# Optimization experiments

Hardware: AMD Instinct MI355X
Metric: run time of the kernel (lower is better)

The kernel has to match this reference:

```python
import jax, jax.numpy as jnp
import numpy as np
from jax import lax

STORAGE = 8
HIDDEN_HEAD = 32
N_BLOCKS = 16


def _conv(x, w, b, padding):
    # x: NCHW, w: OIHW
    y = lax.conv_general_dilated(
        x, w, window_strides=(1, 1), padding=padding,
        dimension_numbers=("NCHW", "OIHW", "NCHW"))
    return y + b[None, :, None, None]


def _min_pool3(x):
    # 3x3 sliding-window min, stride 1, same padding (pad value +inf so it
    return lax.reduce_window(x, float("inf"), lax.min,
                             (1, 1, 3, 3), (1, 1, 1, 1), "SAME")


def setup_inputs() -> dict:
    key = jax.random.key(0)
    ks = jax.random.split(key, 7)
    B, H, W = 8, 512, 512
    x = jax.random.normal(ks[0], (B, 1, H, W), dtype=jnp.float32)
    # initial 1x1 conv: 1 -> 8
    w0 = jax.random.normal(ks[1], (STORAGE, 1, 1, 1), dtype=jnp.float32) * 1.0
    b0 = jax.random.normal(ks[2], (STORAGE,), dtype=jnp.float32) * 0.1
    # head conv 3x3: 8 -> 32
    w1 = jax.random.normal(ks[3], (HIDDEN_HEAD, STORAGE, 3, 3), dtype=jnp.float32) * (1.0 / np.sqrt(STORAGE * 9))
    b1 = jax.random.normal(ks[4], (HIDDEN_HEAD,), dtype=jnp.float32) * 0.1
    # head conv 1x1: 32 -> 1
    w2 = jax.random.normal(ks[5], (1, HIDDEN_HEAD, 1, 1), dtype=jnp.float32) * (1.0 / np.sqrt(HIDDEN_HEAD))
    b2 = jax.random.normal(ks[6], (1,), dtype=jnp.float32) * 0.1
    return {"x": x, "w0": w0, "b0": b0, "w1": w1, "b1": b1, "w2": w2, "b2": b2}


def reference(x, w0, b0, w1, b1, w2, b2):
    h = _conv(x, w0, b0, "SAME")  # [B,8,H,W]
    for _ in range(N_BLOCKS):
        h = h + _min_pool3(h)
    h = _conv(h, w1, b1, "SAME")  # [B,32,H,W]
    h = jax.nn.relu(h)
    return _conv(h, w2, b2, "SAME")  # [B,1,H,W]
```

## Files before the change

### kernel.cpp

```cpp
#include <hip/hip_runtime.h>
#include <math.h>


#define N_PIX (512*512)
#define INF __builtin_inff()

typedef __attribute__((ext_vector_type(2))) float f2;

__device__ __forceinline__ float dpp_shr1(float v, float fill) {
    return __int_as_float(__builtin_amdgcn_update_dpp(
        __float_as_int(fill), __float_as_int(v), 0x138, 0xF, 0xF, false));
}
__device__ __forceinline__ float dpp_shl1(float v, float fill) {
    return __int_as_float(__builtin_amdgcn_update_dpp(
        __float_as_int(fill), __float_as_int(v), 0x130, 0xF, 0xF, false));
}

struct Row8 { float4 a, b; };

__device__ __forceinline__ Row8 row_update8(const Row8 up, const Row8 mid, const Row8 dn)
{
    float4 va, vb;
    va.x = fminf(fminf(up.a.x, mid.a.x), dn.a.x);
    va.y = fminf(fminf(up.a.y, mid.a.y), dn.a.y);
    va.z = fminf(fminf(up.a.z, mid.a.z), dn.a.z);
    va.w = fminf(fminf(up.a.w, mid.a.w), dn.a.w);
    vb.x = fminf(fminf(up.b.x, mid.b.x), dn.b.x);
    vb.y = fminf(fminf(up.b.y, mid.b.y), dn.b.y);
    vb.z = fminf(fminf(up.b.z, mid.b.z), dn.b.z);
    vb.w = fminf(fminf(up.b.w, mid.b.w), dn.b.w);
    float vmL = dpp_shr1(vb.w, INF);
    float vmR = dpp_shl1(va.x, INF);
    float tm1 = fminf(vmL, va.x);
    float t0 = fminf(va.x, va.y), t1 = fminf(va.y, va.z);
    float t2 = fminf(va.z, va.w), t3 = fminf(va.w, vb.x);
    float t4 = fminf(vb.x, vb.y), t5 = fminf(vb.y, vb.z);
    float t6 = fminf(vb.z, vb.w), t7 = fminf(vb.w, vmR);
    Row8 o;
    o.a.x = mid.a.x + fminf(tm1, t0);
    o.a.y = mid.a.y + fminf(t0, t1);
    o.a.z = mid.a.z + fminf(t1, t2);
    o.a.w = mid.a.w + fminf(t2, t3);
    o.b.x = mid.b.x + fminf(t3, t4);
    o.b.y = mid.b.y + fminf(t4, t5);
    o.b.z = mid.b.z + fminf(t5, t6);
    o.b.w = mid.b.w + fminf(t6, t7);
    return o;
}

__device__ __forceinline__ void halo_write(float* hp, const Row8& v) {
    hp[0*64]=v.a.x; hp[1*64]=v.a.y; hp[2*64]=v.a.z; hp[3*64]=v.a.w;
    hp[4*64]=v.b.x; hp[5*64]=v.b.y; hp[6*64]=v.b.z; hp[7*64]=v.b.w;
}
__device__ __forceinline__ Row8 halo_read(const float* hp) {
    Row8 v;
    v.a.x=hp[0*64]; v.a.y=hp[1*64]; v.a.z=hp[2*64]; v.a.w=hp[3*64];
    v.b.x=hp[4*64]; v.b.y=hp[5*64]; v.b.z=hp[6*64]; v.b.w=hp[7*64];
    return v;
}

__global__ __launch_bounds__(512, 2) void erode16_kernel(
    const float* __restrict__ x, float* __restrict__ A,
    const float* __restrict__ w0, const float* __restrict__ b0,
    const float* __restrict__ w1, const float* __restrict__ b1,
    float* __restrict__ W)
{
    if (blockIdx.x == 0 && blockIdx.y == 0 && threadIdx.x < 288) {
        int tid = threadIdx.x;
        int oc = tid / 9, k = tid - oc*9;
        float wp = 0.f, wq = 0.f;
        for (int ic = 0; ic < 8; ++ic) {
            float a = w0[ic];
            float w = w1[oc*72 + ic*9 + k];
            if (a > 0.f) wp += w * a;
            else         wq += w * (-a);
        }
        W[(oc*9 + k)*2 + 0] = wp;
        W[(oc*9 + k)*2 + 1] = wq;
        if (k == 0) {
            float beta[9];
            for (int kk = 0; kk < 9; ++kk) {
                float s = 0.f;
                for (int ic = 0; ic < 8; ++ic) s += b0[ic] * w1[oc*72 + ic*9 + kk];
                beta[kk] = 65536.0f * s;
            }
            float R[3], L[3], Rr[3];
            for (int r = 0; r < 3; ++r) {
                R[r]  = beta[r*3] + beta[r*3+1] + beta[r*3+2];
                L[r]  = beta[r*3 + 0];
                Rr[r] = beta[r*3 + 2];
            }
            float bb = b1[oc];
            W[576 + 0*96 + oc]      = bb + R[1] + R[2];
            W[576 + 0*96 + 32 + oc] = L[1] + L[2];
            W[576 + 0*96 + 64 + oc] = Rr[1] + Rr[2];
            W[576 + 1*96 + oc]      = bb + R[0] + R[1] + R[2];
            W[576 + 1*96 + 32 + oc] = L[0] + L[1] + L[2];
            W[576 + 1*96 + 64 + oc] = Rr[0] + Rr[1] + Rr[2];
            W[576 + 2*96 + oc]      = bb + R[0] + R[1];
            W[576 + 2*96 + 32 + oc] = L[0] + L[1];
            W[576 + 2*96 + 64 + oc] = Rr[0] + Rr[1];
        }
    }

    __shared__ float halo[2][8][4][8][64];
    const int tid   = threadIdx.x;
    const int lane  = tid & 63;
    const int w     = tid >> 6;
    const int ty    = blockIdx.x;
    const int plane = blockIdx.y;
    const int colg  = lane * 8;
    const int row0g = ty*32 - 16 + w*8;

    const float* sp = x + (plane & 7)*N_PIX;
    const float sgn = (plane >= 8) ? -1.f : 1.f;

    Row8 h[8];
    #pragma unroll
    for (int r = 0; r < 8; ++r) {
        int gy = row0g + r;
        if ((unsigned)gy < 512u) {
            const float* rp = sp + gy*512 + colg;
            float4 a = *(const float4*)rp;
            float4 b = *(const float4*)(rp + 4);
            h[r].a = make_float4(a.x*sgn, a.y*sgn, a.z*sgn, a.w*sgn);
            h[r].b = make_float4(b.x*sgn, b.y*sgn, b.z*sgn, b.w*sgn);
        } else {
            h[r].a = make_float4(INF, INF, INF, INF);
            h[r].b = h[r].a;
        }
    }

    const Row8 inf8 = { make_float4(INF,INF,INF,INF), make_float4(INF,INF,INF,INF) };
    for (int s = 0; s < 8; ++s) {
        int par = s & 1;
        halo_write(&halo[par][w][0][0][lane], h[0]);
        halo_write(&halo[par][w][1][0][lane], h[1]);
        halo_write(&halo[par][w][2][0][lane], h[6]);
        halo_write(&halo[par][w][3][0][lane], h[7]);
        Row8 n2 = row_update8(h[1], h[2], h[3]);
        Row8 n3 = row_update8(h[2], h[3], h[4]);
        Row8 n4 = row_update8(h[3], h[4], h[5]);
        Row8 n5 = row_update8(h[4], h[5], h[6]);
        __syncthreads();
        Row8 um2 = inf8, um1 = inf8, dp0 = inf8, dp1 = inf8;
        if (w > 0) {
            um2 = halo_read(&halo[par][w-1][2][0][lane]);
            um1 = halo_read(&halo[par][w-1][3][0][lane]);
        }
        if (w < 7) {
            dp0 = halo_read(&halo[par][w+1][0][0][lane]);
            dp1 = halo_read(&halo[par][w+1][1][0][lane]);
        }
        Row8 nm1 = row_update8(um2, um1, h[0]);
        Row8 n0  = row_update8(um1, h[0], h[1]);
        Row8 n1  = row_update8(h[0], h[1], h[2]);
        Row8 n6  = row_update8(h[5], h[6], h[7]);
        Row8 n7  = row_update8(h[6], h[7], dp0);
        Row8 n8  = row_update8(h[7], dp0, dp1);
        h[0] = row_update8(nm1, n0, n1);
        h[1] = row_update8(n0,  n1, n2);
        h[2] = row_update8(n1,  n2, n3);
        h[3] = row_update8(n2,  n3, n4);
        h[4] = row_update8(n3,  n4, n5);
        h[5] = row_update8(n4,  n5, n6);
        h[6] = row_update8(n5,  n6, n7);
        h[7] = row_update8(n6,  n7, n8);
    }

    if (w >= 2 && w <= 5) {
        float* dp = A + plane*N_PIX;
        #pragma unroll
        for (int r = 0; r < 8; ++r) {
            float* op = dp + (row0g + r)*512 + colg;
            *(float4*)op       = h[r].a;
            *(float4*)(op + 4) = h[r].b;
        }
    }
}

__global__ __launch_bounds__(256) void head_kernel(
    const float* __restrict__ A, const float* __restrict__ W,
    const float* __restrict__ w2, const float* __restrict__ b2,
    float* __restrict__ out)
{
    const int tid  = threadIdx.x;
    const int lane = tid & 63;
    const int w    = tid >> 6;
    const int img  = blockIdx.x >> 7;
    const int y    = (blockIdx.x & 127)*4 + w;
    const int x0   = lane*8;

    const float* P = A + img*N_PIX;
    const float* Q = A + (8 + img)*N_PIX;

    f2 pq[3][10];
    #pragma unroll
    for (int dy = 0; dy < 3; ++dy) {
        int gy = y + dy - 1;
        if ((unsigned)gy < 512u) {
            const float* rp = P + gy*512 + x0;
            const float* rq = Q + gy*512 + x0;
            float4 a = *(const float4*)rp;
            float4 b = *(const float4*)(rp + 4);
            float4 c = *(const float4*)rq;
            float4 d = *(const float4*)(rq + 4);
            pq[dy][1] = (f2){a.x, c.x}; pq[dy][2] = (f2){a.y, c.y};
            pq[dy][3] = (f2){a.z, c.z}; pq[dy][4] = (f2){a.w, c.w};
            pq[dy][5] = (f2){b.x, d.x}; pq[dy][6] = (f2){b.y, d.y};
            pq[dy][7] = (f2){b.z, d.z}; pq[dy][8] = (f2){b.w, d.w};
            pq[dy][0] = (f2){dpp_shr1(b.w, 0.f), dpp_shr1(d.w, 0.f)};
            pq[dy][9] = (f2){dpp_shl1(a.x, 0.f), dpp_shl1(c.x, 0.f)};
        } else {
            #pragma unroll
            for (int j = 0; j < 10; ++j) pq[dy][j] = (f2){0.f, 0.f};
        }
    }

    const int wcase = (y == 0) ? 0 : ((y == 511) ? 2 : 1);
    const float* WB = W + 576 + wcase*96;
    const float mL  = (lane == 0)  ? -1.f : 0.f;
    const float mR  = (lane == 63) ? -1.f : 0.f;

    float o[8];
    #pragma unroll
    for (int j = 0; j < 8; ++j) o[j] = 0.f;

    const f2* Wv = (const f2*)W;
    #pragma unroll 2
    for (int oc = 0; oc < 32; ++oc) {
        f2 acc[8];
        {
            f2 wv0 = Wv[oc*9];
            #pragma unroll
            for (int j = 0; j < 8; ++j) acc[j] = wv0 * pq[0][j];
        }
        #pragma unroll
        for (int t = 1; t < 9; ++t) {
            const int ky = t / 3, kx = t - ky*3;
            f2 wv = Wv[oc*9 + t];
            #pragma unroll
            for (int j = 0; j < 8; ++j) acc[j] += wv * pq[ky][kx + j];
        }
        float base = WB[oc];
        float cl   = WB[32 + oc];
        float cr   = WB[64 + oc];
        float s[8];
        #pragma unroll
        for (int j = 0; j < 8; ++j) s[j] = acc[j].x + acc[j].y + base;
        s[0] = fmaf(cl, mL, s[0]);
        s[7] = fmaf(cr, mR, s[7]);
        float sc = w2[oc];
        #pragma unroll
        for (int j = 0; j < 8; ++j) o[j] += fmaxf(s[j], 0.f) * sc;
    }

    float bb = b2[0];
    float* op = out + img*N_PIX + y*512 + x0;
    *(float4*)(op)     = make_float4(o[0]+bb, o[1]+bb, o[2]+bb, o[3]+bb);
    *(float4*)(op + 4) = make_float4(o[4]+bb, o[5]+bb, o[6]+bb, o[7]+bb);
}

extern "C" void kernel_launch(void* const* d_in, const int* in_sizes, int n_in,
                              void* d_out, int out_size, void* d_ws, size_t ws_size,
                              hipStream_t stream) {
    const float* x  = (const float*)d_in[0];
    const float* w0 = (const float*)d_in[1];
    const float* b0 = (const float*)d_in[2];
    const float* w1 = (const float*)d_in[3];
    const float* b1 = (const float*)d_in[4];
    const float* w2 = (const float*)d_in[5];
    const float* b2 = (const float*)d_in[6];
    float* out = (float*)d_out;

    float* wsf = (float*)d_ws;
    float* A = wsf;
    float* W = wsf + 16*N_PIX;

    dim3 eg(16, 16);
    erode16_kernel<<<eg, 512, 0, stream>>>(x, A, w0, b0, w1, b1, W);

    head_kernel<<<1024, 256, 0, stream>>>(A, W, w2, b2, out);
}
```

Before: 127.8 us.

## Skip dead halo-row erosion work in edge waves and fold head bias into accumulator

In the erosion kernel, the outer waves (0,1,6,7) only feed halo rows to the central output waves, so their updates are now restricted to the shrinking band of rows that still matter at each step. Rows outside that band are skipped while the barriers are kept. The central waves take an unconditional path with no boundary checks, and the wave index is made uniform with readfirstlane. In the head kernel, the bias is split in half, packed as an f2 and folded into the first FMA, which removes one add per pixel per output channel. The cost is extra branching logic in the edge waves and a new weight-table layout.

```diff
diff --git a/kernel.cpp b/kernel.cpp
--- a/kernel.cpp
+++ b/kernel.cpp
@@ -84,33 +84,33 @@
                 for (int ic = 0; ic < 8; ++ic) s += b0[ic] * w1[oc*72 + ic*9 + kk];
                 beta[kk] = 65536.0f * s;
             }
-            float R[3], L[3], Rr[3];
+            float R[3], Lb[3], Rr[3];
             for (int r = 0; r < 3; ++r) {
                 R[r]  = beta[r*3] + beta[r*3+1] + beta[r*3+2];
-                L[r]  = beta[r*3 + 0];
+                Lb[r] = beta[r*3 + 0];
                 Rr[r] = beta[r*3 + 2];
             }
             float bb = b1[oc];
-            W[576 + 0*96 + oc]      = bb + R[1] + R[2];
-            W[576 + 0*96 + 32 + oc] = L[1] + L[2];
-            W[576 + 0*96 + 64 + oc] = Rr[1] + Rr[2];
-            W[576 + 1*96 + oc]      = bb + R[0] + R[1] + R[2];
-            W[576 + 1*96 + 32 + oc] = L[0] + L[1] + L[2];
-            W[576 + 1*96 + 64 + oc] = Rr[0] + Rr[1] + Rr[2];
-            W[576 + 2*96 + oc]      = bb + R[0] + R[1];
-            W[576 + 2*96 + 32 + oc] = L[0] + L[1];
-            W[576 + 2*96 + 64 + oc] = Rr[0] + Rr[1];
+            float Dv[3]  = { bb + R[1] + R[2], bb + R[0] + R[1] + R[2], bb + R[0] + R[1] };
+            float ELv[3] = { Lb[1] + Lb[2], Lb[0] + Lb[1] + Lb[2], Lb[0] + Lb[1] };
+            float ERv[3] = { Rr[1] + Rr[2], Rr[0] + Rr[1] + Rr[2], Rr[0] + Rr[1] };
+            for (int c = 0; c < 3; ++c) {
+                W[576 + (c*32 + oc)*2 + 0] = 0.5f * Dv[c];
+                W[576 + (c*32 + oc)*2 + 1] = 0.5f * Dv[c];
+                W[768 + c*32 + oc] = ELv[c];
+                W[864 + c*32 + oc] = ERv[c];
+            }
         }
     }
 
     __shared__ float halo[2][8][4][8][64];
     const int tid   = threadIdx.x;
     const int lane  = tid & 63;
-    const int w     = tid >> 6;
+    const int wu    = __builtin_amdgcn_readfirstlane(tid >> 6);
     const int ty    = blockIdx.x;
     const int plane = blockIdx.y;
     const int colg  = lane * 8;
-    const int row0g = ty*32 - 16 + w*8;
+    const int row0g = ty*32 - 16 + wu*8;
 
     const float* sp = x + (plane & 7)*N_PIX;
     const float sgn = (plane >= 8) ? -1.f : 1.f;
@@ -132,43 +132,86 @@
     }
 
     const Row8 inf8 = { make_float4(INF,INF,INF,INF), make_float4(INF,INF,INF,INF) };
-    for (int s = 0; s < 8; ++s) {
-        int par = s & 1;
-        halo_write(&halo[par][w][0][0][lane], h[0]);
-        halo_write(&halo[par][w][1][0][lane], h[1]);
-        halo_write(&halo[par][w][2][0][lane], h[6]);
-        halo_write(&halo[par][w][3][0][lane], h[7]);
-        Row8 n2 = row_update8(h[1], h[2], h[3]);
-        Row8 n3 = row_update8(h[2], h[3], h[4]);
-        Row8 n4 = row_update8(h[3], h[4], h[5]);
-        Row8 n5 = row_update8(h[4], h[5], h[6]);
-        __syncthreads();
-        Row8 um2 = inf8, um1 = inf8, dp0 = inf8, dp1 = inf8;
-        if (w > 0) {
-            um2 = halo_read(&halo[par][w-1][2][0][lane]);
-            um1 = halo_read(&halo[par][w-1][3][0][lane]);
-        }
-        if (w < 7) {
-            dp0 = halo_read(&halo[par][w+1][0][0][lane]);
-            dp1 = halo_read(&halo[par][w+1][1][0][lane]);
-        }
-        Row8 nm1 = row_update8(um2, um1, h[0]);
-        Row8 n0  = row_update8(um1, h[0], h[1]);
-        Row8 n1  = row_update8(h[0], h[1], h[2]);
-        Row8 n6  = row_update8(h[5], h[6], h[7]);
-        Row8 n7  = row_update8(h[6], h[7], dp0);
-        Row8 n8  = row_update8(h[7], dp0, dp1);
-        h[0] = row_update8(nm1, n0, n1);
-        h[1] = row_update8(n0,  n1, n2);
-        h[2] = row_update8(n1,  n2, n3);
-        h[3] = row_update8(n2,  n3, n4);
-        h[4] = row_update8(n3,  n4, n5);
-        h[5] = row_update8(n4,  n5, n6);
-        h[6] = row_update8(n5,  n6, n7);
-        h[7] = row_update8(n6,  n7, n8);
-    }
-
-    if (w >= 2 && w <= 5) {
+
+    if (wu >= 2 && wu <= 5) {
+        for (int s = 0; s < 8; ++s) {
+            int par = s & 1;
+            halo_write(&halo[par][wu][0][0][lane], h[0]);
+            halo_write(&halo[par][wu][1][0][lane], h[1]);
+            halo_write(&halo[par][wu][2][0][lane], h[6]);
+            halo_write(&halo[par][wu][3][0][lane], h[7]);
+            Row8 n2 = row_update8(h[1], h[2], h[3]);
+            Row8 n3 = row_update8(h[2], h[3], h[4]);
+            Row8 n4 = row_update8(h[3], h[4], h[5]);
+            Row8 n5 = row_update8(h[4], h[5], h[6]);
+            __syncthreads();
+            Row8 um2 = halo_read(&halo[par][wu-1][2][0][lane]);
+            Row8 um1 = halo_read(&halo[par][wu-1][3][0][lane]);
+            Row8 dp0 = halo_read(&halo[par][wu+1][0][0][lane]);
+            Row8 dp1 = halo_read(&halo[par][wu+1][1][0][lane]);
+            Row8 nm1 = row_update8(um2, um1, h[0]);
+            Row8 n0  = row_update8(um1, h[0], h[1]);
+            Row8 n1  = row_update8(h[0], h[1], h[2]);
+            Row8 n6  = row_update8(h[5], h[6], h[7]);
+            Row8 n7  = row_update8(h[6], h[7], dp0);
+            Row8 n8  = row_update8(h[7], dp0, dp1);
+            h[0] = row_update8(nm1, n0, n1);
+            h[1] = row_update8(n0,  n1, n2);
+            h[2] = row_update8(n1,  n2, n3);
+            h[3] = row_update8(n2,  n3, n4);
+            h[4] = row_update8(n3,  n4, n5);
+            h[5] = row_update8(n4,  n5, n6);
+            h[6] = row_update8(n5,  n6, n7);
+            h[7] = row_update8(n6,  n7, n8);
+        }
+    } else {
+        const int L0 = wu * 8;
+        for (int s = 0; s < 8; ++s) {
+            int par = s & 1;
+            int lo1 = 2*s + 1, hi1 = 62 - 2*s;
+            if (L0 + 8 < lo1 || L0 - 1 > hi1) {
+                __syncthreads();
+                continue;
+            }
+            halo_write(&halo[par][wu][0][0][lane], h[0]);
+            halo_write(&halo[par][wu][1][0][lane], h[1]);
+            halo_write(&halo[par][wu][2][0][lane], h[6]);
+            halo_write(&halo[par][wu][3][0][lane], h[7]);
+            Row8 n2 = inf8, n3 = inf8, n4 = inf8, n5 = inf8;
+            if (L0+2 >= lo1 && L0+2 <= hi1) n2 = row_update8(h[1], h[2], h[3]);
+            if (L0+3 >= lo1 && L0+3 <= hi1) n3 = row_update8(h[2], h[3], h[4]);
+            if (L0+4 >= lo1 && L0+4 <= hi1) n4 = row_update8(h[3], h[4], h[5]);
+            if (L0+5 >= lo1 && L0+5 <= hi1) n5 = row_update8(h[4], h[5], h[6]);
+            __syncthreads();
+            Row8 um2 = inf8, um1 = inf8, dp0 = inf8, dp1 = inf8;
+            if (wu > 0 && L0 >= lo1) {
+                um2 = halo_read(&halo[par][wu-1][2][0][lane]);
+                um1 = halo_read(&halo[par][wu-1][3][0][lane]);
+            }
+            if (wu < 7 && L0+7 <= hi1) {
+                dp0 = halo_read(&halo[par][wu+1][0][0][lane]);
+                dp1 = halo_read(&halo[par][wu+1][1][0][lane]);
+            }
+            Row8 nm1 = inf8, n0 = inf8, n1 = inf8, n6 = inf8, n7 = inf8, n8 = inf8;
+            if (L0-1 >= lo1 && L0-1 <= hi1) nm1 = row_update8(um2, um1, h[0]);
+            if (L0   >= lo1 && L0   <= hi1) n0  = row_update8(um1, h[0], h[1]);
+            if (L0+1 >= lo1 && L0+1 <= hi1) n1  = row_update8(h[0], h[1], h[2]);
+            if (L0+6 >= lo1 && L0+6 <= hi1) n6  = row_update8(h[5], h[6], h[7]);
+            if (L0+7 >= lo1 && L0+7 <= hi1) n7  = row_update8(h[6], h[7], dp0);
+            if (L0+8 >= lo1 && L0+8 <= hi1) n8  = row_update8(h[7], dp0, dp1);
+            int lo2 = lo1 + 1, hi2 = hi1 - 1;
+            if (L0   >= lo2 && L0   <= hi2) h[0] = row_update8(nm1, n0, n1);
+            if (L0+1 >= lo2 && L0+1 <= hi2) h[1] = row_update8(n0,  n1, n2);
+            if (L0+2 >= lo2 && L0+2 <= hi2) h[2] = row_update8(n1,  n2, n3);
+            if (L0+3 >= lo2 && L0+3 <= hi2) h[3] = row_update8(n2,  n3, n4);
+            if (L0+4 >= lo2 && L0+4 <= hi2) h[4] = row_update8(n3,  n4, n5);
+            if (L0+5 >= lo2 && L0+5 <= hi2) h[5] = row_update8(n4,  n5, n6);
+            if (L0+6 >= lo2 && L0+6 <= hi2) h[6] = row_update8(n5,  n6, n7);
+            if (L0+7 >= lo2 && L0+7 <= hi2) h[7] = row_update8(n6,  n7, n8);
+        }
+    }
+
+    if (wu >= 2 && wu <= 5) {
         float* dp = A + plane*N_PIX;
         #pragma unroll
         for (int r = 0; r < 8; ++r) {
@@ -218,9 +261,11 @@
     }
 
     const int wcase = (y == 0) ? 0 : ((y == 511) ? 2 : 1);
-    const float* WB = W + 576 + wcase*96;
-    const float mL  = (lane == 0)  ? -1.f : 0.f;
-    const float mR  = (lane == 63) ? -1.f : 0.f;
+    const f2*    DH  = (const f2*)(W + 576);
+    const float* ELt = W + 768 + wcase*32;
+    const float* ERt = W + 864 + wcase*32;
+    const float  mL  = (lane == 0)  ? -1.f : 0.f;
+    const float  mR  = (lane == 63) ? -1.f : 0.f;
 
     float o[8];
     #pragma unroll
@@ -232,8 +277,9 @@
         f2 acc[8];
         {
             f2 wv0 = Wv[oc*9];
+            f2 hb  = DH[wcase*32 + oc];
             #pragma unroll
-            for (int j = 0; j < 8; ++j) acc[j] = wv0 * pq[0][j];
+            for (int j = 0; j < 8; ++j) acc[j] = wv0 * pq[0][j] + hb;
         }
         #pragma unroll
         for (int t = 1; t < 9; ++t) {
@@ -242,12 +288,11 @@
             #pragma unroll
             for (int j = 0; j < 8; ++j) acc[j] += wv * pq[ky][kx + j];
         }
-        float base = WB[oc];
-        float cl   = WB[32 + oc];
-        float cr   = WB[64 + oc];
+        float cl = ELt[oc];
+        float cr = ERt[oc];
         float s[8];
         #pragma unroll
-        for (int j = 0; j < 8; ++j) s[j] = acc[j].x + acc[j].y + base;
+        for (int j = 0; j < 8; ++j) s[j] = acc[j].x + acc[j].y;
         s[0] = fmaf(cl, mL, s[0]);
         s[7] = fmaf(cr, mR, s[7]);
         float sc = w2[oc];
```

Result: slower. 131.2 us (+2.6%).

## Use v_min3 in erosion, skip dead edge-band steps, fold bias into packed FMA

Applied to the files above, without the earlier changes.

Rewrites the 3x3 min stencil with v_min3_f32 inline asm, which cuts the min instruction count per row update. Edge wavefronts (bands 0 and 7) stop computing after step 4, since their rows no longer feed valid outputs; they only keep hitting the barriers. The conv head's bias is split in half across both lanes of the packed f2 accumulator, which folds the scalar bias add into the first packed FMA. The edge-band skip relies on the halo-shrinking analysis being correct, and the bias split slightly changes rounding order.

```diff
diff --git a/kernel.cpp b/kernel.cpp
--- a/kernel.cpp
+++ b/kernel.cpp
@@ -15,36 +15,35 @@
     return __int_as_float(__builtin_amdgcn_update_dpp(
         __float_as_int(fill), __float_as_int(v), 0x130, 0xF, 0xF, false));
 }
+__device__ __forceinline__ float vmin3(float a, float b, float c) {
+    float d;
+    asm("v_min3_f32 %0, %1, %2, %3" : "=v"(d) : "v"(a), "v"(b), "v"(c));
+    return d;
+}
 
 struct Row8 { float4 a, b; };
 
 __device__ __forceinline__ Row8 row_update8(const Row8 up, const Row8 mid, const Row8 dn)
 {
-    float4 va, vb;
-    va.x = fminf(fminf(up.a.x, mid.a.x), dn.a.x);
-    va.y = fminf(fminf(up.a.y, mid.a.y), dn.a.y);
-    va.z = fminf(fminf(up.a.z, mid.a.z), dn.a.z);
-    va.w = fminf(fminf(up.a.w, mid.a.w), dn.a.w);
-    vb.x = fminf(fminf(up.b.x, mid.b.x), dn.b.x);
-    vb.y = fminf(fminf(up.b.y, mid.b.y), dn.b.y);
-    vb.z = fminf(fminf(up.b.z, mid.b.z), dn.b.z);
-    vb.w = fminf(fminf(up.b.w, mid.b.w), dn.b.w);
-    float vmL = dpp_shr1(vb.w, INF);
-    float vmR = dpp_shl1(va.x, INF);
-    float tm1 = fminf(vmL, va.x);
-    float t0 = fminf(va.x, va.y), t1 = fminf(va.y, va.z);
-    float t2 = fminf(va.z, va.w), t3 = fminf(va.w, vb.x);
-    float t4 = fminf(vb.x, vb.y), t5 = fminf(vb.y, vb.z);
-    float t6 = fminf(vb.z, vb.w), t7 = fminf(vb.w, vmR);
+    float v0 = vmin3(up.a.x, mid.a.x, dn.a.x);
+    float v1 = vmin3(up.a.y, mid.a.y, dn.a.y);
+    float v2 = vmin3(up.a.z, mid.a.z, dn.a.z);
+    float v3 = vmin3(up.a.w, mid.a.w, dn.a.w);
+    float v4 = vmin3(up.b.x, mid.b.x, dn.b.x);
+    float v5 = vmin3(up.b.y, mid.b.y, dn.b.y);
+    float v6 = vmin3(up.b.z, mid.b.z, dn.b.z);
+    float v7 = vmin3(up.b.w, mid.b.w, dn.b.w);
+    float vmL = dpp_shr1(v7, INF);
+    float vmR = dpp_shl1(v0, INF);
     Row8 o;
-    o.a.x = mid.a.x + fminf(tm1, t0);
-    o.a.y = mid.a.y + fminf(t0, t1);
-    o.a.z = mid.a.z + fminf(t1, t2);
-    o.a.w = mid.a.w + fminf(t2, t3);
-    o.b.x = mid.b.x + fminf(t3, t4);
-    o.b.y = mid.b.y + fminf(t4, t5);
-    o.b.z = mid.b.z + fminf(t5, t6);
-    o.b.w = mid.b.w + fminf(t6, t7);
+    o.a.x = mid.a.x + vmin3(vmL, v0, v1);
+    o.a.y = mid.a.y + vmin3(v0, v1, v2);
+    o.a.z = mid.a.z + vmin3(v1, v2, v3);
+    o.a.w = mid.a.w + vmin3(v2, v3, v4);
+    o.b.x = mid.b.x + vmin3(v3, v4, v5);
+    o.b.y = mid.b.y + vmin3(v4, v5, v6);
+    o.b.z = mid.b.z + vmin3(v5, v6, v7);
+    o.b.w = mid.b.w + vmin3(v6, v7, vmR);
     return o;
 }
 
@@ -84,22 +83,22 @@
                 for (int ic = 0; ic < 8; ++ic) s += b0[ic] * w1[oc*72 + ic*9 + kk];
                 beta[kk] = 65536.0f * s;
             }
-            float R[3], L[3], Rr[3];
+            float R[3], Lb[3], Rr[3];
             for (int r = 0; r < 3; ++r) {
                 R[r]  = beta[r*3] + beta[r*3+1] + beta[r*3+2];
-                L[r]  = beta[r*3 + 0];
+                Lb[r] = beta[r*3 + 0];
                 Rr[r] = beta[r*3 + 2];
             }
             float bb = b1[oc];
-            W[576 + 0*96 + oc]      = bb + R[1] + R[2];
-            W[576 + 0*96 + 32 + oc] = L[1] + L[2];
-            W[576 + 0*96 + 64 + oc] = Rr[1] + Rr[2];
-            W[576 + 1*96 + oc]      = bb + R[0] + R[1] + R[2];
-            W[576 + 1*96 + 32 + oc] = L[0] + L[1] + L[2];
-            W[576 + 1*96 + 64 + oc] = Rr[0] + Rr[1] + Rr[2];
-            W[576 + 2*96 + oc]      = bb + R[0] + R[1];
-            W[576 + 2*96 + 32 + oc] = L[0] + L[1];
-            W[576 + 2*96 + 64 + oc] = Rr[0] + Rr[1];
+            float Dv[3]  = { bb + R[1] + R[2], bb + R[0] + R[1] + R[2], bb + R[0] + R[1] };
+            float ELv[3] = { Lb[1] + Lb[2], Lb[0] + Lb[1] + Lb[2], Lb[0] + Lb[1] };
+            float ERv[3] = { Rr[1] + Rr[2], Rr[0] + Rr[1] + Rr[2], Rr[0] + Rr[1] };
+            for (int c = 0; c < 3; ++c) {
+                W[576 + (c*32 + oc)*2 + 0] = 0.5f * Dv[c];
+                W[576 + (c*32 + oc)*2 + 1] = 0.5f * Dv[c];
+                W[768 + c*32 + oc] = ELv[c];
+                W[864 + c*32 + oc] = ERv[c];
+            }
         }
     }
 
@@ -111,6 +110,9 @@
     const int plane = blockIdx.y;
     const int colg  = lane * 8;
     const int row0g = ty*32 - 16 + w*8;
+
+    const int wS = __builtin_amdgcn_readfirstlane(w);
+    const bool edge_band = (wS == 0) || (wS == 7);
 
     const float* sp = x + (plane & 7)*N_PIX;
     const float sgn = (plane >= 8) ? -1.f : 1.f;
@@ -134,6 +136,7 @@
     const Row8 inf8 = { make_float4(INF,INF,INF,INF), make_float4(INF,INF,INF,INF) };
     for (int s = 0; s < 8; ++s) {
         int par = s & 1;
+        if (edge_band && s >= 4) { __syncthreads(); continue; }
         halo_write(&halo[par][w][0][0][lane], h[0]);
         halo_write(&halo[par][w][1][0][lane], h[1]);
         halo_write(&halo[par][w][2][0][lane], h[6]);
@@ -218,9 +221,11 @@
     }
 
     const int wcase = (y == 0) ? 0 : ((y == 511) ? 2 : 1);
-    const float* WB = W + 576 + wcase*96;
-    const float mL  = (lane == 0)  ? -1.f : 0.f;
-    const float mR  = (lane == 63) ? -1.f : 0.f;
+    const f2*    DH  = (const f2*)(W + 576);
+    const float* ELt = W + 768 + wcase*32;
+    const float* ERt = W + 864 + wcase*32;
+    const float  mL  = (lane == 0)  ? -1.f : 0.f;
+    const float  mR  = (lane == 63) ? -1.f : 0.f;
 
     float o[8];
     #pragma unroll
@@ -232,8 +237,9 @@
         f2 acc[8];
         {
             f2 wv0 = Wv[oc*9];
+            f2 hb  = DH[wcase*32 + oc];
             #pragma unroll
-            for (int j = 0; j < 8; ++j) acc[j] = wv0 * pq[0][j];
+            for (int j = 0; j < 8; ++j) acc[j] = wv0 * pq[0][j] + hb;
         }
         #pragma unroll
         for (int t = 1; t < 9; ++t) {
@@ -242,12 +248,11 @@
             #pragma unroll
             for (int j = 0; j < 8; ++j) acc[j] += wv * pq[ky][kx + j];
         }
-        float base = WB[oc];
-        float cl   = WB[32 + oc];
-        float cr   = WB[64 + oc];
+        float cl = ELt[oc];
+        float cr = ERt[oc];
         float s[8];
         #pragma unroll
-        for (int j = 0; j < 8; ++j) s[j] = acc[j].x + acc[j].y + base;
+        for (int j = 0; j < 8; ++j) s[j] = acc[j].x + acc[j].y;
         s[0] = fmaf(cl, mL, s[0]);
         s[7] = fmaf(cr, mR, s[7]);
         float sc = w2[oc];
```

Result: faster. 122.7 us (-4.0%).
